# Optimization experiments

Hardware: AMD Instinct MI355X
Metric: run time of the kernel (lower is better)

Reference implementation:

```python
import jax, jax.numpy as jnp
import numpy as np

N_HEAD = 8
D_Q = 1024
D_K = 1024  # d_k_original
DK = D_K // N_HEAD  # per-head dim = 128
B = 64
L = 2048


def setup_inputs() -> dict:
    key = jax.random.key(0)
    ks = jax.random.split(key, 8)
    std_q = np.sqrt(2.0 / (D_Q + DK)).astype(np.float32)
    std_k = np.sqrt(2.0 / (D_K + DK)).astype(np.float32)
    return {
        "q": jax.random.normal(ks[0], (B, D_Q), jnp.float32),
        "k": jax.random.normal(ks[1], (B, L, D_K), jnp.float32),
        "mask": jnp.zeros((B, L), jnp.bool_),
        # Linear weights stored torch-style: (out_features, in_features)
        "w_qs_w": jax.random.normal(ks[2], (N_HEAD * DK, D_Q), jnp.float32) * std_q,
        "w_qs_b": jnp.zeros((N_HEAD * DK,), jnp.float32),
        "w_ks_w": jax.random.normal(ks[3], (N_HEAD * DK, D_K), jnp.float32) * std_k,
        "w_ks_b": jnp.zeros((N_HEAD * DK,), jnp.float32),
        "w_vs_w": jax.random.normal(ks[4], (N_HEAD * DK, D_K), jnp.float32) * std_k,
        "w_vs_b": jnp.zeros((N_HEAD * DK,), jnp.float32),
    }


def reference(q, k, mask, w_qs_w, w_qs_b, w_ks_w, w_ks_b, w_vs_w, w_vs_b):
    # Dropouts are identity (eval mode).
    b, l, _ = k.shape
    temperature = jnp.sqrt(jnp.asarray(DK, q.dtype))
    # Projections: torch Linear y = x @ W.T + b
    qs = (q @ w_qs_w.T + w_qs_b).reshape(b, N_HEAD, DK)          # (b, n, dk)
    ks = (k @ w_ks_w.T + w_ks_b).reshape(b, l, N_HEAD, DK)       # (b, l, n, dk)
    vs = (k @ w_vs_w.T + w_vs_b).reshape(b, l, N_HEAD, DK)       # (b, l, n, dv)
    # Single-query per head attention scores: (b, n, l)
    attn = jnp.einsum("bnd,blnd->bnl", qs, ks) / temperature
    attn = jnp.where(mask[:, None, :], -jnp.inf, attn)
    attn = jax.nn.softmax(attn, axis=-1)
    # Weighted sum over l: (b, n, dv) -> (b, n*dv)
    output = jnp.einsum("bnl,blnd->bnd", attn, vs).reshape(b, N_HEAD * DK)
    # attn returned head-major like original: (n*b, l)
    attn_out = attn.transpose(1, 0, 2).reshape(N_HEAD * b, l)
    return (output, attn_out)
```

## Files before the change

kernel.cpp:

```cpp
#include <hip/hip_runtime.h>
#include <hip/hip_bf16.h>
#include <math.h>

#define B 64
#define L 2048
#define C 1024
#define NH 8
#define DK 128
#define SCALE 0.08838834764831845f

__global__ void k_qs(const float* __restrict__ q, const float* __restrict__ wq,
                     const float* __restrict__ bq, float* __restrict__ qs) {
    int t = threadIdx.x, w = t >> 6, lane = t & 63;
    int j = blockIdx.x * 4 + w;
    float4 W[4];
#pragma unroll
    for (int kk = 0; kk < 4; kk++)
        W[kk] = *(const float4*)&wq[(size_t)j * C + kk * 256 + lane * 4];
    float bj = bq[j];
    for (int b = 0; b < B; b++) {
        float s = 0.f;
#pragma unroll
        for (int kk = 0; kk < 4; kk++) {
            float4 qv = *(const float4*)&q[(size_t)b * C + kk * 256 + lane * 4];
            s += W[kk].x * qv.x + W[kk].y * qv.y + W[kk].z * qv.z + W[kk].w * qv.w;
        }
#pragma unroll
        for (int off = 32; off; off >>= 1) s += __shfl_xor(s, off, 64);
        if (lane == 0) qs[(size_t)b * C + j] = s + bj;
    }
}

__global__ void k_qtilde(const float* __restrict__ qs, const float* __restrict__ wk,
                         float* __restrict__ qtilde) {
    int n = blockIdx.x >> 2, cc = blockIdx.x & 3, bg = blockIdx.y;
    int t = threadIdx.x;
    int c = cc * 256 + t;
    __shared__ float qss[8][128];
    for (int p = 0; p < 4; p++) {
        int e = p * 256 + t;
        int i = e >> 7, d = e & 127;
        qss[i][d] = qs[(size_t)(bg * 8 + i) * C + n * DK + d];
    }
    __syncthreads();
    float acc[8];
#pragma unroll
    for (int i = 0; i < 8; i++) acc[i] = 0.f;
    for (int d = 0; d < DK; d++) {
        float wv = wk[(size_t)(n * DK + d) * C + c];
#pragma unroll
        for (int i = 0; i < 8; i++) acc[i] += qss[i][d] * wv;
    }
#pragma unroll
    for (int i = 0; i < 8; i++)
        qtilde[((size_t)(bg * 8 + i) * NH + n) * C + c] = acc[i] * SCALE;
}

__global__ __launch_bounds__(512, 2) void k_fused4(
    const float* __restrict__ kmat, const float* __restrict__ qtilde,
    const unsigned char* __restrict__ mask,
    float* __restrict__ pout,
    float* __restrict__ accpart,
    float* __restrict__ zpart) {
    const int b = blockIdx.x, lp = blockIdx.y;
    const int t = threadIdx.x, w = t >> 6, lane = t & 63;
    const int chunk = w >> 1;
    const int hg = w & 1;
    const int l0 = lp * 512 + chunk * 128;
    const int hl = lane & 3;

    __shared__ float ctxl[NH * C];
    __shared__ float zl[NH];

    float4 qt[4][4];
#pragma unroll
    for (int j = 0; j < 4; j++)
#pragma unroll
        for (int kk = 0; kk < 4; kk++)
            qt[j][kk] = *(const float4*)&qtilde[((size_t)b * NH + hg * 4 + j) * C + kk * 256 + lane * 4];

    float4 acc[4][4];
#pragma unroll
    for (int j = 0; j < 4; j++)
#pragma unroll
        for (int kk = 0; kk < 4; kk++) acc[j][kk] = make_float4(0.f, 0.f, 0.f, 0.f);
    float zacc = 0.f;

    const float* kp = kmat + ((size_t)b * L + l0) * C + lane * 4;
    const unsigned char* mp = mask + (size_t)b * L + l0;

    float4 kv[4][4];
#pragma unroll
    for (int kk = 0; kk < 4; kk++) {
        kv[0][kk] = *(const float4*)(kp + kk * 256);
        kv[1][kk] = *(const float4*)(kp + (size_t)C + kk * 256);
    }

    for (int rb = 0; rb < 32; rb++) {
        uchar4 mb = *(const uchar4*)&mp[rb * 4];
        float ss[4];
#pragma unroll
        for (int rr = 0; rr < 4; rr++) {
            const int r = rb * 4 + rr;
            {
                int lpre = r + 2; if (lpre > 127) lpre = 127;
                const float* np = kp + (size_t)lpre * C;
#pragma unroll
                for (int kk = 0; kk < 4; kk++)
                    kv[(rr + 2) & 3][kk] = *(const float4*)(np + kk * 256);
            }
            float s0 = 0.f, s1 = 0.f, s2 = 0.f, s3 = 0.f;
#pragma unroll
            for (int kk = 0; kk < 4; kk++) {
                float4 kq = kv[rr][kk];
                s0 += qt[0][kk].x * kq.x + qt[0][kk].y * kq.y + qt[0][kk].z * kq.z + qt[0][kk].w * kq.w;
                s1 += qt[1][kk].x * kq.x + qt[1][kk].y * kq.y + qt[1][kk].z * kq.z + qt[1][kk].w * kq.w;
                s2 += qt[2][kk].x * kq.x + qt[2][kk].y * kq.y + qt[2][kk].z * kq.z + qt[2][kk].w * kq.w;
                s3 += qt[3][kk].x * kq.x + qt[3][kk].y * kq.y + qt[3][kk].z * kq.z + qt[3][kk].w * kq.w;
            }
            float a01 = (lane & 1) ? s1 : s0;
            float g01 = (lane & 1) ? s0 : s1;
            float a23 = (lane & 1) ? s3 : s2;
            float g23 = (lane & 1) ? s2 : s3;
            float u  = a01 + __shfl_xor(g01, 1, 64);
            float v2 = a23 + __shfl_xor(g23, 1, 64);
            float keep = (lane & 2) ? v2 : u;
            float give = (lane & 2) ? u : v2;
            float v = keep + __shfl_xor(give, 2, 64);
            v += __shfl_xor(v, 4, 64);
            v += __shfl_xor(v, 8, 64);
            v += __shfl_xor(v, 16, 64);
            v += __shfl_xor(v, 32, 64);
            unsigned char mk = (rr == 0) ? mb.x : (rr == 1) ? mb.y : (rr == 2) ? mb.z : mb.w;
            float p = __expf(mk ? -INFINITY : v);
            zacc += p;
            ss[rr] = p;
            float p1 = __shfl_xor(p, 1, 64);
            float p2 = __shfl_xor(p, 2, 64);
            float p3 = __shfl_xor(p1, 2, 64);
#pragma unroll
            for (int kk = 0; kk < 4; kk++) {
                float4 kq = kv[rr][kk];
                acc[0][kk].x += p  * kq.x; acc[0][kk].y += p  * kq.y; acc[0][kk].z += p  * kq.z; acc[0][kk].w += p  * kq.w;
                acc[1][kk].x += p1 * kq.x; acc[1][kk].y += p1 * kq.y; acc[1][kk].z += p1 * kq.z; acc[1][kk].w += p1 * kq.w;
                acc[2][kk].x += p2 * kq.x; acc[2][kk].y += p2 * kq.y; acc[2][kk].z += p2 * kq.z; acc[2][kk].w += p2 * kq.w;
                acc[3][kk].x += p3 * kq.x; acc[3][kk].y += p3 * kq.y; acc[3][kk].z += p3 * kq.z; acc[3][kk].w += p3 * kq.w;
            }
        }
        if (lane < 4) {
            float4 o = make_float4(ss[0], ss[1], ss[2], ss[3]);
            *(float4*)&pout[((size_t)(hg * 4 + lane) * B + b) * L + l0 + rb * 4] = o;
        }
    }

    __syncthreads();
    for (int ph = 0; ph < 4; ph++) {
        if (chunk == ph) {
#pragma unroll
            for (int j = 0; j < 4; j++) {
                int h = hg * 4 + (hl ^ j);
                float* dst = &ctxl[(size_t)h * C + lane * 4];
                if (ph == 0) {
#pragma unroll
                    for (int kk = 0; kk < 4; kk++)
                        *(float4*)&dst[kk * 256] = acc[j][kk];
                } else {
#pragma unroll
                    for (int kk = 0; kk < 4; kk++) {
                        float4 o = *(const float4*)&dst[kk * 256];
                        float4 a = acc[j][kk];
                        o.x += a.x; o.y += a.y; o.z += a.z; o.w += a.w;
                        *(float4*)&dst[kk * 256] = o;
                    }
                }
            }
            if (lane < 4) {
                if (ph == 0) zl[hg * 4 + lane] = zacc;
                else         zl[hg * 4 + lane] += zacc;
            }
        }
        __syncthreads();
    }
    float* ap = accpart + ((size_t)b * 4 + lp) * (NH * C);
#pragma unroll
    for (int i = 0; i < 4; i++) {
        int idx = t * 16 + i * 4;
        *(float4*)&ap[idx] = *(const float4*)&ctxl[idx];
    }
    if (t < NH) zpart[((size_t)b * 4 + lp) * NH + t] = zl[t];
}

__global__ void k_combine2(const float* __restrict__ accpart, const float* __restrict__ zpart,
                           float* __restrict__ ctx, float* __restrict__ pout) {
    int b = blockIdx.x, cq = blockIdx.y;
    int t = threadIdx.x;
    int c = cq * 256 + t;
    __shared__ float zi[NH];
    if (t < NH) {
        float z = 0.f;
#pragma unroll
        for (int lpp = 0; lpp < 4; lpp++) z += zpart[((size_t)b * 4 + lpp) * NH + t];
        zi[t] = 1.0f / z;
    }
    __syncthreads();
#pragma unroll
    for (int n = 0; n < NH; n++) {
        float s = 0.f;
#pragma unroll
        for (int lpp = 0; lpp < 4; lpp++)
            s += accpart[(((size_t)b * 4 + lpp) * NH + n) * C + c];
        ctx[((size_t)b * NH + n) * C + c] = s * zi[n];
    }
#pragma unroll
    for (int n = 0; n < NH; n++) {
        float zin = zi[n];
        float2* pp = (float2*)&pout[((size_t)n * B + b) * L + cq * 512];
        float2 v = pp[t];
        v.x *= zin; v.y *= zin;
        pp[t] = v;
    }
}

__global__ void k_out(const float* __restrict__ ctx, const float* __restrict__ wv,
                      const float* __restrict__ bv, float* __restrict__ out) {
    int t = threadIdx.x, w = t >> 6, lane = t & 63;
    int j = blockIdx.x * 4 + w;
    int n = j >> 7;
    float4 W[4];
#pragma unroll
    for (int kk = 0; kk < 4; kk++)
        W[kk] = *(const float4*)&wv[(size_t)j * C + kk * 256 + lane * 4];
    float bj = bv[j];
    for (int b = 0; b < B; b++) {
        float s = 0.f;
#pragma unroll
        for (int kk = 0; kk < 4; kk++) {
            float4 cv = *(const float4*)&ctx[((size_t)b * NH + n) * C + kk * 256 + lane * 4];
            s += W[kk].x * cv.x + W[kk].y * cv.y + W[kk].z * cv.z + W[kk].w * cv.w;
        }
#pragma unroll
        for (int off = 32; off; off >>= 1) s += __shfl_xor(s, off, 64);
        if (lane == 0) out[(size_t)b * (NH * DK) + j] = s + bj;
    }
}

extern "C" void kernel_launch(void* const* d_in, const int* in_sizes, int n_in,
                              void* d_out, int out_size, void* d_ws, size_t ws_size,
                              hipStream_t stream) {
    const float* q    = (const float*)d_in[0];
    const float* kmat = (const float*)d_in[1];
    const unsigned char* mask = (const unsigned char*)d_in[2];
    const float* wq = (const float*)d_in[3];
    const float* bq = (const float*)d_in[4];
    const float* wk = (const float*)d_in[5];
    const float* wv = (const float*)d_in[7];
    const float* bv = (const float*)d_in[8];

    float* out  = (float*)d_out;
    float* attn = out + B * NH * DK;

    float* ws      = (float*)d_ws;
    float* qs      = ws;
    float* zpart   = ws;
    float* qtilde  = ws + 65536;
    float* ctx     = qtilde;
    float* accpart = ws + 65536 + 524288;

    hipLaunchKernelGGL(k_qs, dim3(256), dim3(256), 0, stream, q, wq, bq, qs);
    hipLaunchKernelGGL(k_qtilde, dim3(32, 8), dim3(256), 0, stream, qs, wk, qtilde);
    hipLaunchKernelGGL(k_fused4, dim3(64, 4), dim3(512), 0, stream,
                       kmat, qtilde, mask, attn, accpart, zpart);
    hipLaunchKernelGGL(k_combine2, dim3(64, 4), dim3(256), 0, stream,
                       accpart, zpart, ctx, attn);
    hipLaunchKernelGGL(k_out, dim3(256), dim3(256), 0, stream, ctx, wv, bv, out);
}
```

Before: 275.7 us.

## Stage K rows through double-buffered shared memory shared by both head groups

Before, the two waves that handle the same rows for different head groups each loaded those K rows from global memory. Now each wave loads one row per 8-row group into a double-buffered LDS tile, and every wave reads its 2 rows back from LDS. The aim is to halve global K traffic and overlap the next group's load with compute. In exchange it adds a block-wide barrier per 8 rows, 64KB more LDS (which may limit the intended 2 blocks per CU), and scalar per-row mask loads and pout stores in place of vectorised ones.

Measured after the change: 259.8 us. -5.8%, faster.

```diff
diff --git a/kernel.cpp b/kernel.cpp
--- a/kernel.cpp
+++ b/kernel.cpp
@@ -56,7 +56,7 @@
         qtilde[((size_t)(bg * 8 + i) * NH + n) * C + c] = acc[i] * SCALE;
 }
 
-__global__ __launch_bounds__(512, 2) void k_fused4(
+__global__ __launch_bounds__(512, 2) void k_fused5(
     const float* __restrict__ kmat, const float* __restrict__ qtilde,
     const unsigned char* __restrict__ mask,
     float* __restrict__ pout,
@@ -64,11 +64,12 @@
     float* __restrict__ zpart) {
     const int b = blockIdx.x, lp = blockIdx.y;
     const int t = threadIdx.x, w = t >> 6, lane = t & 63;
-    const int chunk = w >> 1;
     const int hg = w & 1;
-    const int l0 = lp * 512 + chunk * 128;
+    const int widx = w >> 1;
+    const int l_base = lp * 512;
     const int hl = lane & 3;
 
+    __shared__ float kbuf[2 * 8 * 1024];
     __shared__ float ctxl[NH * C];
     __shared__ float zl[NH];
 
@@ -86,33 +87,48 @@
         for (int kk = 0; kk < 4; kk++) acc[j][kk] = make_float4(0.f, 0.f, 0.f, 0.f);
     float zacc = 0.f;
 
-    const float* kp = kmat + ((size_t)b * L + l0) * C + lane * 4;
-    const unsigned char* mp = mask + (size_t)b * L + l0;
-
-    float4 kv[4][4];
-#pragma unroll
-    for (int kk = 0; kk < 4; kk++) {
-        kv[0][kk] = *(const float4*)(kp + kk * 256);
-        kv[1][kk] = *(const float4*)(kp + (size_t)C + kk * 256);
-    }
-
-    for (int rb = 0; rb < 32; rb++) {
-        uchar4 mb = *(const uchar4*)&mp[rb * 4];
-        float ss[4];
-#pragma unroll
-        for (int rr = 0; rr < 4; rr++) {
-            const int r = rb * 4 + rr;
-            {
-                int lpre = r + 2; if (lpre > 127) lpre = 127;
-                const float* np = kp + (size_t)lpre * C;
-#pragma unroll
-                for (int kk = 0; kk < 4; kk++)
-                    kv[(rr + 2) & 3][kk] = *(const float4*)(np + kk * 256);
-            }
+    const float* kgbase = kmat + ((size_t)b * L + l_base) * C + lane * 4;
+    const unsigned char* mp = mask + (size_t)b * L + l_base;
+
+    {
+        const float* gp = kgbase + (size_t)w * C;
+        float4 s0 = *(const float4*)(gp);
+        float4 s1 = *(const float4*)(gp + 256);
+        float4 s2 = *(const float4*)(gp + 512);
+        float4 s3 = *(const float4*)(gp + 768);
+        float* dst = &kbuf[w * 1024 + lane * 4];
+        *(float4*)(dst)       = s0;
+        *(float4*)(dst + 256) = s1;
+        *(float4*)(dst + 512) = s2;
+        *(float4*)(dst + 768) = s3;
+    }
+    __syncthreads();
+
+    for (int g = 0; g < 64; g++) {
+        float4 sreg[4];
+        const bool has_next = (g < 63);
+        if (has_next) {
+            const float* gp = kgbase + (size_t)((g + 1) * 8 + w) * C;
+#pragma unroll
+            for (int kk = 0; kk < 4; kk++)
+                sreg[kk] = *(const float4*)(gp + kk * 256);
+        }
+
+        const int l0 = g * 8 + 2 * widx;
+        const float* kb0 = &kbuf[(g & 1) * 8192 + (2 * widx) * 1024 + lane * 4];
+        float4 kvr[2][4];
+#pragma unroll
+        for (int rr = 0; rr < 2; rr++)
+#pragma unroll
+            for (int kk = 0; kk < 4; kk++)
+                kvr[rr][kk] = *(const float4*)&kb0[rr * 1024 + kk * 256];
+
+#pragma unroll
+        for (int rr = 0; rr < 2; rr++) {
             float s0 = 0.f, s1 = 0.f, s2 = 0.f, s3 = 0.f;
 #pragma unroll
             for (int kk = 0; kk < 4; kk++) {
-                float4 kq = kv[rr][kk];
+                float4 kq = kvr[rr][kk];
                 s0 += qt[0][kk].x * kq.x + qt[0][kk].y * kq.y + qt[0][kk].z * kq.z + qt[0][kk].w * kq.w;
                 s1 += qt[1][kk].x * kq.x + qt[1][kk].y * kq.y + qt[1][kk].z * kq.z + qt[1][kk].w * kq.w;
                 s2 += qt[2][kk].x * kq.x + qt[2][kk].y * kq.y + qt[2][kk].z * kq.z + qt[2][kk].w * kq.w;
@@ -131,31 +147,35 @@
             v += __shfl_xor(v, 8, 64);
             v += __shfl_xor(v, 16, 64);
             v += __shfl_xor(v, 32, 64);
-            unsigned char mk = (rr == 0) ? mb.x : (rr == 1) ? mb.y : (rr == 2) ? mb.z : mb.w;
+            unsigned char mk = mp[l0 + rr];
             float p = __expf(mk ? -INFINITY : v);
             zacc += p;
-            ss[rr] = p;
+            if (lane < 4)
+                pout[((size_t)(hg * 4 + lane) * B + b) * L + l_base + l0 + rr] = p;
             float p1 = __shfl_xor(p, 1, 64);
             float p2 = __shfl_xor(p, 2, 64);
             float p3 = __shfl_xor(p1, 2, 64);
 #pragma unroll
             for (int kk = 0; kk < 4; kk++) {
-                float4 kq = kv[rr][kk];
+                float4 kq = kvr[rr][kk];
                 acc[0][kk].x += p  * kq.x; acc[0][kk].y += p  * kq.y; acc[0][kk].z += p  * kq.z; acc[0][kk].w += p  * kq.w;
                 acc[1][kk].x += p1 * kq.x; acc[1][kk].y += p1 * kq.y; acc[1][kk].z += p1 * kq.z; acc[1][kk].w += p1 * kq.w;
                 acc[2][kk].x += p2 * kq.x; acc[2][kk].y += p2 * kq.y; acc[2][kk].z += p2 * kq.z; acc[2][kk].w += p2 * kq.w;
                 acc[3][kk].x += p3 * kq.x; acc[3][kk].y += p3 * kq.y; acc[3][kk].z += p3 * kq.z; acc[3][kk].w += p3 * kq.w;
             }
         }
-        if (lane < 4) {
-            float4 o = make_float4(ss[0], ss[1], ss[2], ss[3]);
-            *(float4*)&pout[((size_t)(hg * 4 + lane) * B + b) * L + l0 + rb * 4] = o;
-        }
-    }
-
-    __syncthreads();
+
+        if (has_next) {
+            float* dst = &kbuf[((g + 1) & 1) * 8192 + w * 1024 + lane * 4];
+#pragma unroll
+            for (int kk = 0; kk < 4; kk++)
+                *(float4*)&dst[kk * 256] = sreg[kk];
+        }
+        __syncthreads();
+    }
+
     for (int ph = 0; ph < 4; ph++) {
-        if (chunk == ph) {
+        if (widx == ph) {
 #pragma unroll
             for (int j = 0; j < 4; j++) {
                 int h = hg * 4 + (hl ^ j);
@@ -268,7 +288,7 @@
 
     hipLaunchKernelGGL(k_qs, dim3(256), dim3(256), 0, stream, q, wq, bq, qs);
     hipLaunchKernelGGL(k_qtilde, dim3(32, 8), dim3(256), 0, stream, qs, wk, qtilde);
-    hipLaunchKernelGGL(k_fused4, dim3(64, 4), dim3(512), 0, stream,
+    hipLaunchKernelGGL(k_fused5, dim3(64, 4), dim3(512), 0, stream,
                        kmat, qtilde, mask, attn, accpart, zpart);
     hipLaunchKernelGGL(k_combine2, dim3(64, 4), dim3(256), 0, stream,
                        accpart, zpart, ctx, attn);
```

## Split heads across more waves, double L-partitions, fuse combine and output projection

Applied to the files above, without the earlier changes.

The main attention kernel now gives each wave 2 heads instead of 4 and doubles the L-partitions per batch (grid 64x8), cutting registers so launch bounds can request 4 blocks per SM. The register prefetch ring for K rows is dropped in favour of direct loads, and a per-iteration __syncthreads is added, which looks unnecessary. The combine and output-projection kernels are merged into one per-batch epilogue that reduces the partials into shared memory, applies the Wv projection and rescales attn. This saves a launch and the ctx round trip, but the epilogue runs only 64 blocks and re-reads Wv once per batch.

New measurement: 656.2 us. +138.0%, slower.

```diff
diff --git a/kernel.cpp b/kernel.cpp
--- a/kernel.cpp
+++ b/kernel.cpp
@@ -56,7 +56,7 @@
         qtilde[((size_t)(bg * 8 + i) * NH + n) * C + c] = acc[i] * SCALE;
 }
 
-__global__ __launch_bounds__(512, 2) void k_fused4(
+__global__ __launch_bounds__(512, 4) void k_fused6(
     const float* __restrict__ kmat, const float* __restrict__ qtilde,
     const unsigned char* __restrict__ mask,
     float* __restrict__ pout,
@@ -64,69 +64,52 @@
     float* __restrict__ zpart) {
     const int b = blockIdx.x, lp = blockIdx.y;
     const int t = threadIdx.x, w = t >> 6, lane = t & 63;
-    const int chunk = w >> 1;
-    const int hg = w & 1;
-    const int l0 = lp * 512 + chunk * 128;
-    const int hl = lane & 3;
+    const int hp = w & 3;
+    const int rh = w >> 2;
+    const int lbase = lp * 256 + rh * 128;
 
     __shared__ float ctxl[NH * C];
     __shared__ float zl[NH];
 
-    float4 qt[4][4];
-#pragma unroll
-    for (int j = 0; j < 4; j++)
+    float4 qt[2][4];
+#pragma unroll
+    for (int j = 0; j < 2; j++)
 #pragma unroll
         for (int kk = 0; kk < 4; kk++)
-            qt[j][kk] = *(const float4*)&qtilde[((size_t)b * NH + hg * 4 + j) * C + kk * 256 + lane * 4];
-
-    float4 acc[4][4];
-#pragma unroll
-    for (int j = 0; j < 4; j++)
+            qt[j][kk] = *(const float4*)&qtilde[((size_t)b * NH + hp * 2 + j) * C + kk * 256 + lane * 4];
+
+    float4 acc[2][4];
+#pragma unroll
+    for (int j = 0; j < 2; j++)
 #pragma unroll
         for (int kk = 0; kk < 4; kk++) acc[j][kk] = make_float4(0.f, 0.f, 0.f, 0.f);
     float zacc = 0.f;
 
-    const float* kp = kmat + ((size_t)b * L + l0) * C + lane * 4;
-    const unsigned char* mp = mask + (size_t)b * L + l0;
-
-    float4 kv[4][4];
-#pragma unroll
-    for (int kk = 0; kk < 4; kk++) {
-        kv[0][kk] = *(const float4*)(kp + kk * 256);
-        kv[1][kk] = *(const float4*)(kp + (size_t)C + kk * 256);
-    }
+    const float* kp = kmat + ((size_t)b * L + lbase) * C + lane * 4;
+    const unsigned char* mp = mask + (size_t)b * L + lbase;
 
     for (int rb = 0; rb < 32; rb++) {
         uchar4 mb = *(const uchar4*)&mp[rb * 4];
         float ss[4];
 #pragma unroll
         for (int rr = 0; rr < 4; rr++) {
-            const int r = rb * 4 + rr;
-            {
-                int lpre = r + 2; if (lpre > 127) lpre = 127;
-                const float* np = kp + (size_t)lpre * C;
-#pragma unroll
-                for (int kk = 0; kk < 4; kk++)
-                    kv[(rr + 2) & 3][kk] = *(const float4*)(np + kk * 256);
-            }
-            float s0 = 0.f, s1 = 0.f, s2 = 0.f, s3 = 0.f;
-#pragma unroll
-            for (int kk = 0; kk < 4; kk++) {
-                float4 kq = kv[rr][kk];
-                s0 += qt[0][kk].x * kq.x + qt[0][kk].y * kq.y + qt[0][kk].z * kq.z + qt[0][kk].w * kq.w;
-                s1 += qt[1][kk].x * kq.x + qt[1][kk].y * kq.y + qt[1][kk].z * kq.z + qt[1][kk].w * kq.w;
-                s2 += qt[2][kk].x * kq.x + qt[2][kk].y * kq.y + qt[2][kk].z * kq.z + qt[2][kk].w * kq.w;
-                s3 += qt[3][kk].x * kq.x + qt[3][kk].y * kq.y + qt[3][kk].z * kq.z + qt[3][kk].w * kq.w;
-            }
-            float a01 = (lane & 1) ? s1 : s0;
-            float g01 = (lane & 1) ? s0 : s1;
-            float a23 = (lane & 1) ? s3 : s2;
-            float g23 = (lane & 1) ? s2 : s3;
-            float u  = a01 + __shfl_xor(g01, 1, 64);
-            float v2 = a23 + __shfl_xor(g23, 1, 64);
-            float keep = (lane & 2) ? v2 : u;
-            float give = (lane & 2) ? u : v2;
-            float v = keep + __shfl_xor(give, 2, 64);
+            const float* rp = kp + (size_t)(rb * 4 + rr) * C;
+            float4 kv0 = *(const float4*)(rp);
+            float4 kv1 = *(const float4*)(rp + 256);
+            float4 kv2 = *(const float4*)(rp + 512);
+            float4 kv3 = *(const float4*)(rp + 768);
+            float s0 = qt[0][0].x * kv0.x + qt[0][0].y * kv0.y + qt[0][0].z * kv0.z + qt[0][0].w * kv0.w
+                     + qt[0][1].x * kv1.x + qt[0][1].y * kv1.y + qt[0][1].z * kv1.z + qt[0][1].w * kv1.w
+                     + qt[0][2].x * kv2.x + qt[0][2].y * kv2.y + qt[0][2].z * kv2.z + qt[0][2].w * kv2.w
+                     + qt[0][3].x * kv3.x + qt[0][3].y * kv3.y + qt[0][3].z * kv3.z + qt[0][3].w * kv3.w;
+            float s1 = qt[1][0].x * kv0.x + qt[1][0].y * kv0.y + qt[1][0].z * kv0.z + qt[1][0].w * kv0.w
+                     + qt[1][1].x * kv1.x + qt[1][1].y * kv1.y + qt[1][1].z * kv1.z + qt[1][1].w * kv1.w
+                     + qt[1][2].x * kv2.x + qt[1][2].y * kv2.y + qt[1][2].z * kv2.z + qt[1][2].w * kv2.w
+                     + qt[1][3].x * kv3.x + qt[1][3].y * kv3.y + qt[1][3].z * kv3.z + qt[1][3].w * kv3.w;
+            float keep = (lane & 1) ? s1 : s0;
+            float give = (lane & 1) ? s0 : s1;
+            float v = keep + __shfl_xor(give, 1, 64);
+            v += __shfl_xor(v, 2, 64);
             v += __shfl_xor(v, 4, 64);
             v += __shfl_xor(v, 8, 64);
             v += __shfl_xor(v, 16, 64);
@@ -136,29 +119,27 @@
             zacc += p;
             ss[rr] = p;
             float p1 = __shfl_xor(p, 1, 64);
-            float p2 = __shfl_xor(p, 2, 64);
-            float p3 = __shfl_xor(p1, 2, 64);
-#pragma unroll
-            for (int kk = 0; kk < 4; kk++) {
-                float4 kq = kv[rr][kk];
-                acc[0][kk].x += p  * kq.x; acc[0][kk].y += p  * kq.y; acc[0][kk].z += p  * kq.z; acc[0][kk].w += p  * kq.w;
-                acc[1][kk].x += p1 * kq.x; acc[1][kk].y += p1 * kq.y; acc[1][kk].z += p1 * kq.z; acc[1][kk].w += p1 * kq.w;
-                acc[2][kk].x += p2 * kq.x; acc[2][kk].y += p2 * kq.y; acc[2][kk].z += p2 * kq.z; acc[2][kk].w += p2 * kq.w;
-                acc[3][kk].x += p3 * kq.x; acc[3][kk].y += p3 * kq.y; acc[3][kk].z += p3 * kq.z; acc[3][kk].w += p3 * kq.w;
-            }
-        }
-        if (lane < 4) {
+            acc[0][0].x += p  * kv0.x; acc[0][0].y += p  * kv0.y; acc[0][0].z += p  * kv0.z; acc[0][0].w += p  * kv0.w;
+            acc[0][1].x += p  * kv1.x; acc[0][1].y += p  * kv1.y; acc[0][1].z += p  * kv1.z; acc[0][1].w += p  * kv1.w;
+            acc[0][2].x += p  * kv2.x; acc[0][2].y += p  * kv2.y; acc[0][2].z += p  * kv2.z; acc[0][2].w += p  * kv2.w;
+            acc[0][3].x += p  * kv3.x; acc[0][3].y += p  * kv3.y; acc[0][3].z += p  * kv3.z; acc[0][3].w += p  * kv3.w;
+            acc[1][0].x += p1 * kv0.x; acc[1][0].y += p1 * kv0.y; acc[1][0].z += p1 * kv0.z; acc[1][0].w += p1 * kv0.w;
+            acc[1][1].x += p1 * kv1.x; acc[1][1].y += p1 * kv1.y; acc[1][1].z += p1 * kv1.z; acc[1][1].w += p1 * kv1.w;
+            acc[1][2].x += p1 * kv2.x; acc[1][2].y += p1 * kv2.y; acc[1][2].z += p1 * kv2.z; acc[1][2].w += p1 * kv2.w;
+            acc[1][3].x += p1 * kv3.x; acc[1][3].y += p1 * kv3.y; acc[1][3].z += p1 * kv3.z; acc[1][3].w += p1 * kv3.w;
+        }
+        if (lane < 2) {
             float4 o = make_float4(ss[0], ss[1], ss[2], ss[3]);
-            *(float4*)&pout[((size_t)(hg * 4 + lane) * B + b) * L + l0 + rb * 4] = o;
-        }
-    }
-
-    __syncthreads();
-    for (int ph = 0; ph < 4; ph++) {
-        if (chunk == ph) {
-#pragma unroll
-            for (int j = 0; j < 4; j++) {
-                int h = hg * 4 + (hl ^ j);
+            *(float4*)&pout[((size_t)(hp * 2 + lane) * B + b) * L + lbase + rb * 4] = o;
+        }
+        __syncthreads();
+    }
+
+    for (int ph = 0; ph < 2; ph++) {
+        if (rh == ph) {
+#pragma unroll
+            for (int j = 0; j < 2; j++) {
+                int h = hp * 2 + ((lane & 1) ^ j);
                 float* dst = &ctxl[(size_t)h * C + lane * 4];
                 if (ph == 0) {
 #pragma unroll
@@ -174,73 +155,78 @@
                     }
                 }
             }
-            if (lane < 4) {
-                if (ph == 0) zl[hg * 4 + lane] = zacc;
-                else         zl[hg * 4 + lane] += zacc;
+            if (lane < 2) {
+                if (ph == 0) zl[hp * 2 + lane] = zacc;
+                else         zl[hp * 2 + lane] += zacc;
             }
         }
         __syncthreads();
     }
-    float* ap = accpart + ((size_t)b * 4 + lp) * (NH * C);
+    float* ap = accpart + ((size_t)b * 8 + lp) * (NH * C);
 #pragma unroll
     for (int i = 0; i < 4; i++) {
         int idx = t * 16 + i * 4;
         *(float4*)&ap[idx] = *(const float4*)&ctxl[idx];
     }
-    if (t < NH) zpart[((size_t)b * 4 + lp) * NH + t] = zl[t];
-}
-
-__global__ void k_combine2(const float* __restrict__ accpart, const float* __restrict__ zpart,
-                           float* __restrict__ ctx, float* __restrict__ pout) {
-    int b = blockIdx.x, cq = blockIdx.y;
-    int t = threadIdx.x;
-    int c = cq * 256 + t;
+    if (t < NH) zpart[((size_t)b * 8 + lp) * NH + t] = zl[t];
+}
+
+__global__ __launch_bounds__(1024) void k_epilogue(
+    const float* __restrict__ accpart, const float* __restrict__ zpart,
+    const float* __restrict__ wvw, const float* __restrict__ bv,
+    float* __restrict__ pout, float* __restrict__ out) {
+    const int b = blockIdx.x;
+    const int t = threadIdx.x;
+    __shared__ float ctxl[NH * C];
     __shared__ float zi[NH];
     if (t < NH) {
         float z = 0.f;
 #pragma unroll
-        for (int lpp = 0; lpp < 4; lpp++) z += zpart[((size_t)b * 4 + lpp) * NH + t];
+        for (int lp = 0; lp < 8; lp++) z += zpart[((size_t)b * 8 + lp) * NH + t];
         zi[t] = 1.0f / z;
     }
     __syncthreads();
 #pragma unroll
-    for (int n = 0; n < NH; n++) {
-        float s = 0.f;
-#pragma unroll
-        for (int lpp = 0; lpp < 4; lpp++)
-            s += accpart[(((size_t)b * 4 + lpp) * NH + n) * C + c];
-        ctx[((size_t)b * NH + n) * C + c] = s * zi[n];
-    }
-#pragma unroll
-    for (int n = 0; n < NH; n++) {
-        float zin = zi[n];
-        float2* pp = (float2*)&pout[((size_t)n * B + b) * L + cq * 512];
-        float2 v = pp[t];
-        v.x *= zin; v.y *= zin;
-        pp[t] = v;
-    }
-}
-
-__global__ void k_out(const float* __restrict__ ctx, const float* __restrict__ wv,
-                      const float* __restrict__ bv, float* __restrict__ out) {
-    int t = threadIdx.x, w = t >> 6, lane = t & 63;
-    int j = blockIdx.x * 4 + w;
-    int n = j >> 7;
-    float4 W[4];
-#pragma unroll
-    for (int kk = 0; kk < 4; kk++)
-        W[kk] = *(const float4*)&wv[(size_t)j * C + kk * 256 + lane * 4];
-    float bj = bv[j];
-    for (int b = 0; b < B; b++) {
-        float s = 0.f;
-#pragma unroll
-        for (int kk = 0; kk < 4; kk++) {
-            float4 cv = *(const float4*)&ctx[((size_t)b * NH + n) * C + kk * 256 + lane * 4];
-            s += W[kk].x * cv.x + W[kk].y * cv.y + W[kk].z * cv.z + W[kk].w * cv.w;
-        }
-#pragma unroll
-        for (int off = 32; off; off >>= 1) s += __shfl_xor(s, off, 64);
-        if (lane == 0) out[(size_t)b * (NH * DK) + j] = s + bj;
+    for (int i = 0; i < 2; i++) {
+        int f4 = i * 1024 + t;
+        float4 s = make_float4(0.f, 0.f, 0.f, 0.f);
+#pragma unroll
+        for (int lp = 0; lp < 8; lp++) {
+            float4 a = *(const float4*)&accpart[((size_t)b * 8 + lp) * (NH * C) + f4 * 4];
+            s.x += a.x; s.y += a.y; s.z += a.z; s.w += a.w;
+        }
+        float sc = zi[f4 >> 8];
+        s.x *= sc; s.y *= sc; s.z *= sc; s.w *= sc;
+        *(float4*)&ctxl[f4 * 4] = s;
+    }
+    __syncthreads();
+    {
+        int wv_i = t >> 6, lane = t & 63;
+        for (int jj = 0; jj < 64; jj++) {
+            int j = wv_i * 64 + jj;
+            int n = j >> 7;
+            float s = 0.f;
+#pragma unroll
+            for (int kk = 0; kk < 4; kk++) {
+                float4 W = *(const float4*)&wvw[(size_t)j * C + kk * 256 + lane * 4];
+                float4 cv = *(const float4*)&ctxl[(size_t)n * C + kk * 256 + lane * 4];
+                s += W.x * cv.x + W.y * cv.y + W.z * cv.z + W.w * cv.w;
+            }
+#pragma unroll
+            for (int off = 32; off; off >>= 1) s += __shfl_xor(s, off, 64);
+            if (lane == 0) out[(size_t)b * (NH * DK) + j] = s + bv[j];
+        }
+    }
+    float4* p4 = (float4*)pout;
+#pragma unroll
+    for (int i = 0; i < 4; i++) {
+        int e = i * 1024 + t;
+        int n = e >> 9, off = e & 511;
+        size_t idx = ((size_t)n * B + b) * (L / 4) + off;
+        float4 v = p4[idx];
+        float sc = zi[n];
+        v.x *= sc; v.y *= sc; v.z *= sc; v.w *= sc;
+        p4[idx] = v;
     }
 }
 
@@ -263,14 +249,12 @@
     float* qs      = ws;
     float* zpart   = ws;
     float* qtilde  = ws + 65536;
-    float* ctx     = qtilde;
     float* accpart = ws + 65536 + 524288;
 
     hipLaunchKernelGGL(k_qs, dim3(256), dim3(256), 0, stream, q, wq, bq, qs);
     hipLaunchKernelGGL(k_qtilde, dim3(32, 8), dim3(256), 0, stream, qs, wk, qtilde);
-    hipLaunchKernelGGL(k_fused4, dim3(64, 4), dim3(512), 0, stream,
+    hipLaunchKernelGGL(k_fused6, dim3(64, 8), dim3(512), 0, stream,
                        kmat, qtilde, mask, attn, accpart, zpart);
-    hipLaunchKernelGGL(k_combine2, dim3(64, 4), dim3(256), 0, stream,
-                       accpart, zpart, ctx, attn);
-    hipLaunchKernelGGL(k_out, dim3(256), dim3(256), 0, stream, ctx, wv, bv, out);
-}
+    hipLaunchKernelGGL(k_epilogue, dim3(64), dim3(1024), 0, stream,
+                       accpart, zpart, wv, bv, attn, out);
+}
```
